# Optimization experiments

Hardware: AMD Instinct MI355X
Metric: run time of the kernel (lower is better)

## Reference

```python
import jax, jax.numpy as jnp
import numpy as np

EMBED_DIM = 128
FFN_DIM = 512
N_NODES = 50000
N_EDGES = 800000
LN_EPS = 1e-5


def setup_inputs() -> dict:
    key = jax.random.key(0)
    ks = jax.random.split(key, 8)
    s = 1.0 / np.sqrt(EMBED_DIM)
    return {
        "x": jax.random.normal(ks[0], (N_NODES, EMBED_DIM), jnp.float32),
        "edge_indices": jax.random.randint(ks[1], (2, N_EDGES), 0, N_NODES, dtype=jnp.int32),
        "W_qkv": jax.random.normal(ks[2], (EMBED_DIM, 3 * EMBED_DIM), jnp.float32) * s,
        "b_qkv": jnp.zeros((3 * EMBED_DIM,), jnp.float32),
        "W1": jax.random.normal(ks[3], (EMBED_DIM, FFN_DIM), jnp.float32) * s,
        "b1": jnp.zeros((FFN_DIM,), jnp.float32),
        "W2": jax.random.normal(ks[4], (FFN_DIM, EMBED_DIM), jnp.float32) * (1.0 / np.sqrt(FFN_DIM)),
        "b2": jnp.zeros((EMBED_DIM,), jnp.float32),
        "g1": jnp.ones((EMBED_DIM,), jnp.float32),
        "be1": jnp.zeros((EMBED_DIM,), jnp.float32),
        "g2": jnp.ones((EMBED_DIM,), jnp.float32),
        "be2": jnp.zeros((EMBED_DIM,), jnp.float32),
    }


def _layernorm(x, g, b):
    mu = jnp.mean(x, axis=-1, keepdims=True)
    var = jnp.mean(jnp.square(x - mu), axis=-1, keepdims=True)
    return (x - mu) * jax.lax.rsqrt(var + LN_EPS) * g + b


def _self_attention(x, edge_indices, W_qkv, b_qkv):
    n = x.shape[0]
    scale = x.shape[1] ** (-0.5)
    qkv = x @ W_qkv + b_qkv
    q, k, v = jnp.split(qkv, 3, axis=1)
    src, dst = edge_indices[0], edge_indices[1]  # row (softmax segment), col
    # per-edge logits: [E]
    alpha = jnp.sum(q[src] * k[dst], axis=1) * scale
    # segment (per-row) stable softmax
    m = jax.ops.segment_max(alpha, src, num_segments=n)
    e = jnp.exp(alpha - m[src])
    denom = jax.ops.segment_sum(e, src, num_segments=n)
    w = e / denom[src]  # [E]
    # sparse.mm: out[i] = sum_{(i,j) in E} w_ij * v[j]
    return jax.ops.segment_sum(w[:, None] * v[dst], src, num_segments=n)


def reference(x, edge_indices, W_qkv, b_qkv, W1, b1, W2, b2, g1, be1, g2, be2):
    # norm_first = False (post-norm), dropout = 0
    x = _layernorm(x + _self_attention(x, edge_indices, W_qkv, b_qkv), g1, be1)
    h = jax.nn.relu(x @ W1 + b1) @ W2 + b2
    x = _layernorm(x + h, g2, be2)
    return x
```

## Files before the change

### kernel.cpp

```cpp
#include <hip/hip_runtime.h>
#include <math.h>

#define NN 50000
#define NE 800000
#define ED 128
#define FD 512
#define MAXDEG 64
#define CURS_STRIDE 16
#define QKV_BLOCKS (NN / 16)
#define SCAT_BLOCKS ((NE + 255) / 256)

typedef __attribute__((ext_vector_type(8))) short bf16x8;
typedef __attribute__((ext_vector_type(4))) float f32x4;
typedef _Float16 half2_t __attribute__((ext_vector_type(2)));

static __device__ __forceinline__ float wave_sum(float x) {
#pragma unroll
  for (int off = 32; off > 0; off >>= 1) x += __shfl_xor(x, off, 64);
  return x;
}

static __device__ __forceinline__ unsigned short f2bf(float f) {
  union { float f; unsigned u; } c; c.f = f;
  unsigned r = c.u + 0x7fffu + ((c.u >> 16) & 1u);
  return (unsigned short)(r >> 16);
}

static __device__ __forceinline__ unsigned short f2h(float f) {
  union { _Float16 h; unsigned short u; } c; c.h = (_Float16)f;
  return c.u;
}

static __device__ __forceinline__ half2_t u2h2(unsigned u) {
  union { unsigned u; half2_t h; } c; c.u = u;
  return c.h;
}

#if __has_builtin(__builtin_amdgcn_fdot2)
#define FDOT2(a, b, c) __builtin_amdgcn_fdot2((a), (b), (c), false)
#else
static __device__ __forceinline__ float FDOT2(half2_t a, half2_t b, float c) {
  return (float)a[0] * (float)b[0] + (float)a[1] * (float)b[1] + c;
}
#endif

__global__ void k_prep(const float* __restrict__ Wqkv, const float* __restrict__ W1,
                       const float* __restrict__ W2, unsigned short* __restrict__ WqkvF,
                       unsigned short* __restrict__ W1F, unsigned short* __restrict__ W2F,
                       int* __restrict__ cursor) {
  int idx = blockIdx.x * 256 + threadIdx.x;
  if (idx < NN) cursor[idx * CURS_STRIDE] = 0;
  if (idx < 49152) {
    int j = idx & 7, l = (idx >> 3) & 63, kb = (idx >> 9) & 3, t = idx >> 11;
    int k = kb * 32 + (l >> 4) * 8 + j, n = t * 16 + (l & 15);
    WqkvF[idx] = f2bf(Wqkv[k * 384 + n]);
  }
  {
    int j = idx & 7, l = (idx >> 3) & 63, kb = (idx >> 9) & 3, t = idx >> 11;
    int k = kb * 32 + (l >> 4) * 8 + j, n = t * 16 + (l & 15);
    W1F[idx] = f2bf(W1[k * 512 + n]);
  }
  {
    int j = idx & 7, l = (idx >> 3) & 63, kb = (idx >> 9) & 15, t = idx >> 13;
    int k = kb * 32 + (l >> 4) * 8 + j, n = t * 16 + (l & 15);
    W2F[idx] = f2bf(W2[k * 128 + n]);
  }
}

__global__ __launch_bounds__(256) void k_qkv_scat(
    const float* __restrict__ X, const unsigned short* __restrict__ WqkvF,
    const float* __restrict__ B, unsigned short* __restrict__ q,
    unsigned short* __restrict__ kv, const int* __restrict__ src,
    const int* __restrict__ dst, int* __restrict__ cursor,
    unsigned short* __restrict__ colidx) {
  __shared__ unsigned short xs[16][136];
  const int tid = threadIdx.x;
  if (blockIdx.x & 1) {
    const int e = (blockIdx.x >> 1) * 256 + tid;
    if (e < NE) {
      const int s = src[e];
      const int d = dst[e];
      const int slot = atomicAdd(&cursor[s * CURS_STRIDE], 1);
      if (slot < MAXDEG) colidx[s * MAXDEG + slot] = (unsigned short)d;
    }
    return;
  }
  const int row0 = (blockIdx.x >> 1) * 16;
  for (int idx = tid; idx < 512; idx += 256) {
    int r = idx >> 5, c4 = (idx & 31) << 2;
    float4 val = *(const float4*)&X[(size_t)(row0 + r) * ED + c4];
    xs[r][c4] = f2bf(val.x); xs[r][c4 + 1] = f2bf(val.y);
    xs[r][c4 + 2] = f2bf(val.z); xs[r][c4 + 3] = f2bf(val.w);
  }
  __syncthreads();
  const int wv = tid >> 6, lane = tid & 63;
  const int ln = lane & 15, quad = lane >> 4;
  const int koff = quad * 8;
  bf16x8 a[4];
#pragma unroll
  for (int kb = 0; kb < 4; kb++) a[kb] = *(const bf16x8*)&xs[ln][kb * 32 + koff];
  for (int g = 0; g < 3; g++) {
    const int t0 = wv * 6 + g * 2;
    bf16x8 b[2][4];
#pragma unroll
    for (int j = 0; j < 2; j++)
#pragma unroll
      for (int kb = 0; kb < 4; kb++)
        b[j][kb] = *(const bf16x8*)&WqkvF[(size_t)(((t0 + j) * 4 + kb) * 64 + lane) * 8];
    f32x4 acc[2];
#pragma unroll
    for (int j = 0; j < 2; j++) acc[j] = (f32x4){0.f, 0.f, 0.f, 0.f};
#pragma unroll
    for (int kb = 0; kb < 4; kb++)
#pragma unroll
      for (int j = 0; j < 2; j++)
        acc[j] = __builtin_amdgcn_mfma_f32_16x16x32_bf16(a[kb], b[j][kb], acc[j], 0, 0, 0);
#pragma unroll
    for (int j = 0; j < 2; j++) {
      const int col = (t0 + j) * 16 + ln;
      const float bias = B[col];
      if (col < 128) {
#pragma unroll
        for (int r = 0; r < 4; r++)
          q[(size_t)(row0 + quad * 4 + r) * ED + col] =
              f2h((acc[j][r] + bias) * 0.08838834764831845f);
      } else {
#pragma unroll
        for (int r = 0; r < 4; r++)
          kv[(size_t)(row0 + quad * 4 + r) * 256 + (col - 128)] = f2h(acc[j][r] + bias);
      }
    }
  }
}

template <bool FULL>
static __device__ __forceinline__ void attn_chunk(
    int base, int cnt, int grp, int gl, int lane, const half2_t* qh,
    const unsigned short* __restrict__ kv, const unsigned short* __restrict__ colidx,
    float& l, half2_t* axh) {
  const int C = FULL ? 16 : cnt;
  int colreg = 0;
  if (lane < C) colreg = colidx[base + lane];
  const int itmax = FULL ? 4 : ((C + 3) >> 2);
#pragma unroll(FULL ? 4 : 1)
  for (int it = 0; it < itmax; it++) {
    const int t = it * 4 + grp;
    const bool act = FULL || t < C;
    const int cc = __shfl(colreg, act ? t : 0, 64);
    const unsigned short* row = &kv[(size_t)cc * 256 + gl * 8];
    uint4 kw = *(const uint4*)row;
    uint4 vw = *(const uint4*)(row + 128);
    float dot = FDOT2(qh[0], u2h2(kw.x), 0.f);
    dot = FDOT2(qh[1], u2h2(kw.y), dot);
    dot = FDOT2(qh[2], u2h2(kw.z), dot);
    dot = FDOT2(qh[3], u2h2(kw.w), dot);
    dot += __shfl_xor(dot, 1, 64);
    dot += __shfl_xor(dot, 2, 64);
    dot += __shfl_xor(dot, 4, 64);
    dot += __shfl_xor(dot, 8, 64);
    const float e = act ? __expf(dot) : 0.f;
    l += e;
    const half2_t e2 = {(_Float16)e, (_Float16)e};
    axh[0] += e2 * u2h2(vw.x);
    axh[1] += e2 * u2h2(vw.y);
    axh[2] += e2 * u2h2(vw.z);
    axh[3] += e2 * u2h2(vw.w);
  }
}

__global__ __launch_bounds__(256) void k_attn(
    const unsigned short* __restrict__ q, const unsigned short* __restrict__ kv,
    const float* __restrict__ x, const int* __restrict__ cursor,
    const unsigned short* __restrict__ colidx, unsigned short* __restrict__ attb) {
  const int wv = threadIdx.x >> 6;
  const int lane = threadIdx.x & 63;
  const int grp = lane >> 4, gl = lane & 15;
  const int node = blockIdx.x * 4 + wv;

  half2_t qh[4];
  {
    uint4 qw = *(const uint4*)&q[(size_t)node * ED + gl * 8];
    qh[0] = u2h2(qw.x); qh[1] = u2h2(qw.y);
    qh[2] = u2h2(qw.z); qh[3] = u2h2(qw.w);
  }
  const int cnt0 = cursor[node * CURS_STRIDE];
  const int cnt = cnt0 > MAXDEG ? MAXDEG : cnt0;
  const int b0 = node * MAXDEG;
  float l = 0.f;
  half2_t axh[4] = {};
  int off = 0;
  for (; off + 16 <= cnt; off += 16)
    attn_chunk<true>(b0 + off, 16, grp, gl, lane, qh, kv, colidx, l, axh);
  if (off < cnt)
    attn_chunk<false>(b0 + off, cnt - off, grp, gl, lane, qh, kv, colidx, l, axh);

#pragma unroll
  for (int j = 0; j < 4; j++) {
    union { half2_t h; int i; } c;
    union { int i; half2_t h; } d;
    c.h = axh[j]; d.i = __shfl_xor(c.i, 16, 64); axh[j] += d.h;
    c.h = axh[j]; d.i = __shfl_xor(c.i, 32, 64); axh[j] += d.h;
  }
  l += __shfl_xor(l, 16, 64);
  l += __shfl_xor(l, 32, 64);

  const float inv = (cnt > 0) ? 1.0f / l : 0.f;
  const int d0 = gl * 8 + grp * 2;
  const half2_t s = (grp == 0) ? axh[0] : (grp == 1) ? axh[1] : (grp == 2) ? axh[2] : axh[3];
  float2 xv = *(const float2*)&x[(size_t)node * ED + d0];
  unsigned pk = (unsigned)f2h(xv.x + (float)s[0] * inv) |
                ((unsigned)f2h(xv.y + (float)s[1] * inv) << 16);
  *(unsigned*)&attb[(size_t)node * ED + d0] = pk;
}

__global__ __launch_bounds__(256) void k_ffn_ln2(
    const unsigned short* __restrict__ attb, const unsigned short* __restrict__ W1F,
    const float* __restrict__ b1, const unsigned short* __restrict__ W2F,
    const float* __restrict__ b2, const float* __restrict__ g1,
    const float* __restrict__ be1, const float* __restrict__ g2,
    const float* __restrict__ be2, float* __restrict__ out) {
  __shared__ unsigned short xs[16][136];
  __shared__ unsigned short hs[16][520];
  __shared__ float ysf[16][132];
  float* ys = (float*)&hs[0][0];
  const int row0 = blockIdx.x * 16;
  const int tid = threadIdx.x;
  {
    const int r = tid >> 4, c8 = (tid & 15) << 3;
    uint4 aw = *(const uint4*)&attb[(size_t)(row0 + r) * ED + c8];
    half2_t h0 = u2h2(aw.x), h1 = u2h2(aw.y), h2 = u2h2(aw.z), h3 = u2h2(aw.w);
    ysf[r][c8] = (float)h0[0];     ysf[r][c8 + 1] = (float)h0[1];
    ysf[r][c8 + 2] = (float)h1[0]; ysf[r][c8 + 3] = (float)h1[1];
    ysf[r][c8 + 4] = (float)h2[0]; ysf[r][c8 + 5] = (float)h2[1];
    ysf[r][c8 + 6] = (float)h3[0]; ysf[r][c8 + 7] = (float)h3[1];
  }
  __syncthreads();
  const int wv = tid >> 6, lane = tid & 63;
#pragma unroll
  for (int half = 0; half < 2; half++) {
    const int r = wv * 4 + half * 2 + (lane >> 5);
    const int hd = (lane & 31) << 2;
    float4 vv = *(const float4*)&ysf[r][hd];
    float s4 = vv.x + vv.y + vv.z + vv.w;
#pragma unroll
    for (int off = 16; off > 0; off >>= 1) s4 += __shfl_xor(s4, off, 64);
    const float mean = s4 * (1.f / ED);
    const float dx0 = vv.x - mean, dx1 = vv.y - mean, dx2 = vv.z - mean, dx3 = vv.w - mean;
    float vr = dx0 * dx0 + dx1 * dx1 + dx2 * dx2 + dx3 * dx3;
#pragma unroll
    for (int off = 16; off > 0; off >>= 1) vr += __shfl_xor(vr, off, 64);
    const float rstd = rsqrtf(vr * (1.f / ED) + 1e-5f);
    const float4 gg = *(const float4*)&g1[hd];
    const float4 bb = *(const float4*)&be1[hd];
    const float o0 = dx0 * rstd * gg.x + bb.x;
    const float o1 = dx1 * rstd * gg.y + bb.y;
    const float o2 = dx2 * rstd * gg.z + bb.z;
    const float o3 = dx3 * rstd * gg.w + bb.w;
    xs[r][hd] = f2bf(o0); xs[r][hd + 1] = f2bf(o1);
    xs[r][hd + 2] = f2bf(o2); xs[r][hd + 3] = f2bf(o3);
    *(float4*)&ysf[r][hd] = make_float4(o0, o1, o2, o3);
  }
  __syncthreads();
  const int ln = lane & 15, quad = lane >> 4;
  const int koff = quad * 8;
  bf16x8 a1[4];
#pragma unroll
  for (int kb = 0; kb < 4; kb++) a1[kb] = *(const bf16x8*)&xs[ln][kb * 32 + koff];
  for (int g = 0; g < 4; g++) {
    const int t0 = wv * 8 + g * 2;
    bf16x8 b[2][4];
#pragma unroll
    for (int j = 0; j < 2; j++)
#pragma unroll
      for (int kb = 0; kb < 4; kb++)
        b[j][kb] = *(const bf16x8*)&W1F[(size_t)(((t0 + j) * 4 + kb) * 64 + lane) * 8];
    f32x4 acc[2];
#pragma unroll
    for (int j = 0; j < 2; j++) acc[j] = (f32x4){0.f, 0.f, 0.f, 0.f};
#pragma unroll
    for (int kb = 0; kb < 4; kb++)
#pragma unroll
      for (int j = 0; j < 2; j++)
        acc[j] = __builtin_amdgcn_mfma_f32_16x16x32_bf16(a1[kb], b[j][kb], acc[j], 0, 0, 0);
#pragma unroll
    for (int j = 0; j < 2; j++) {
      const int col = (t0 + j) * 16 + ln;
      const float bias = b1[col];
#pragma unroll
      for (int r = 0; r < 4; r++)
        hs[quad * 4 + r][col] = f2bf(fmaxf(acc[j][r] + bias, 0.f));
    }
  }
  __syncthreads();
  f32x4 acc2[2];
  acc2[0] = (f32x4){0.f, 0.f, 0.f, 0.f};
  acc2[1] = (f32x4){0.f, 0.f, 0.f, 0.f};
  const int nt0 = wv * 2;
  for (int kg = 0; kg < 4; kg++) {
    bf16x8 a[4];
#pragma unroll
    for (int kk = 0; kk < 4; kk++)
      a[kk] = *(const bf16x8*)&hs[ln][(kg * 4 + kk) * 32 + koff];
    bf16x8 b[2][4];
#pragma unroll
    for (int nt = 0; nt < 2; nt++)
#pragma unroll
      for (int kk = 0; kk < 4; kk++)
        b[nt][kk] = *(const bf16x8*)&W2F[(size_t)(((nt0 + nt) * 16 + kg * 4 + kk) * 64 + lane) * 8];
#pragma unroll
    for (int kk = 0; kk < 4; kk++)
#pragma unroll
      for (int nt = 0; nt < 2; nt++)
        acc2[nt] = __builtin_amdgcn_mfma_f32_16x16x32_bf16(a[kk], b[nt][kk], acc2[nt], 0, 0, 0);
  }
  __syncthreads();
#pragma unroll
  for (int nt = 0; nt < 2; nt++) {
    const int col = (nt0 + nt) * 16 + ln;
    const float bias = b2[col];
#pragma unroll
    for (int r = 0; r < 4; r++)
      ys[(quad * 4 + r) * 132 + col] = acc2[nt][r] + bias;
  }
  __syncthreads();
  float2 gg = *(const float2*)&g2[2 * lane];
  float2 bbe = *(const float2*)&be2[2 * lane];
#pragma unroll
  for (int rr = 0; rr < 4; rr++) {
    const int r = wv * 4 + rr;
    const int row = row0 + r;
    float vx = ys[r * 132 + 2 * lane] + ysf[r][2 * lane];
    float vy = ys[r * 132 + 2 * lane + 1] + ysf[r][2 * lane + 1];
    float mean = wave_sum(vx + vy) * (1.f / ED);
    float dx = vx - mean, dy = vy - mean;
    float var = wave_sum(dx * dx + dy * dy) * (1.f / ED);
    float rstd = rsqrtf(var + 1e-5f);
    float2 o = make_float2(dx * rstd * gg.x + bbe.x, dy * rstd * gg.y + bbe.y);
    *(float2*)&out[(size_t)row * ED + 2 * lane] = o;
  }
}

extern "C" void kernel_launch(void* const* d_in, const int* in_sizes, int n_in,
                              void* d_out, int out_size, void* d_ws, size_t ws_size,
                              hipStream_t stream) {
  const float* x = (const float*)d_in[0];
  const int* ei = (const int*)d_in[1];
  const float* W_qkv = (const float*)d_in[2];
  const float* b_qkv = (const float*)d_in[3];
  const float* W1 = (const float*)d_in[4];
  const float* b1 = (const float*)d_in[5];
  const float* W2 = (const float*)d_in[6];
  const float* b2 = (const float*)d_in[7];
  const float* g1 = (const float*)d_in[8];
  const float* be1 = (const float*)d_in[9];
  const float* g2 = (const float*)d_in[10];
  const float* be2 = (const float*)d_in[11];
  float* out = (float*)d_out;

  char* ws = (char*)d_ws;
  size_t off = 0;
  auto alloc = [&](size_t bytes) -> char* {
    char* p = ws + off;
    off = (off + bytes + 255) & ~(size_t)255;
    return p;
  };
  unsigned short* q = (unsigned short*)alloc(2 * (size_t)NN * ED);
  unsigned short* kv = (unsigned short*)alloc(2 * (size_t)NN * 256);
  unsigned short* attb = (unsigned short*)alloc(2 * (size_t)NN * ED);
  unsigned short* WqkvF = (unsigned short*)alloc(2 * 24 * 4 * 64 * 8);
  unsigned short* W1F = (unsigned short*)alloc(2 * 32 * 4 * 64 * 8);
  unsigned short* W2F = (unsigned short*)alloc(2 * 8 * 16 * 64 * 8);
  int* cursor = (int*)alloc(sizeof(int) * (size_t)NN * CURS_STRIDE);
  unsigned short* colidx = (unsigned short*)alloc(sizeof(unsigned short) * (size_t)NN * MAXDEG);

  k_prep<<<256, 256, 0, stream>>>(W_qkv, W1, W2, WqkvF, W1F, W2F, cursor);
  k_qkv_scat<<<QKV_BLOCKS + SCAT_BLOCKS, 256, 0, stream>>>(x, WqkvF, b_qkv, q, kv,
                                                           ei, ei + NE, cursor, colidx);
  k_attn<<<NN / 4, 256, 0, stream>>>(q, kv, x, cursor, colidx, attb);
  k_ffn_ln2<<<NN / 16, 256, 0, stream>>>(attb, W1F, b1, W2F, b2, g1, be1, g2, be2, out);
}
```

Baseline: 235.7 us.

## Fuse sparse attention into FFN/LayerNorm kernel, keep residual in fp16 LDS

Merges the attention kernel into the FFN+LN2 kernel. Each 16-row block now first computes attention for its 16 nodes, four per wave run sequentially, and writes the residual sum directly to shared memory. This removes the intermediate global buffer and one kernel launch. The LN1 output kept for the second residual is now stored in fp16 in LDS instead of fp32, which cuts shared memory but adds rounding. The trade-off is fewer blocks (NN/16 instead of NN/4) with serialized per-node gather work, which lowers occupancy and latency hiding for the irregular gathers.

```diff
diff --git a/kernel.cpp b/kernel.cpp
--- a/kernel.cpp
+++ b/kernel.cpp
@@ -29,6 +29,11 @@
 static __device__ __forceinline__ unsigned short f2h(float f) {
   union { _Float16 h; unsigned short u; } c; c.h = (_Float16)f;
   return c.u;
+}
+
+static __device__ __forceinline__ float h2f(unsigned short u) {
+  union { unsigned short u; _Float16 h; } c; c.u = u;
+  return (float)c.h;
 }
 
 static __device__ __forceinline__ half2_t u2h2(unsigned u) {
@@ -168,84 +173,72 @@
   }
 }
 
-__global__ __launch_bounds__(256) void k_attn(
+__global__ __launch_bounds__(256) void k_attn_ffn(
     const unsigned short* __restrict__ q, const unsigned short* __restrict__ kv,
     const float* __restrict__ x, const int* __restrict__ cursor,
-    const unsigned short* __restrict__ colidx, unsigned short* __restrict__ attb) {
-  const int wv = threadIdx.x >> 6;
-  const int lane = threadIdx.x & 63;
-  const int grp = lane >> 4, gl = lane & 15;
-  const int node = blockIdx.x * 4 + wv;
-
-  half2_t qh[4];
-  {
-    uint4 qw = *(const uint4*)&q[(size_t)node * ED + gl * 8];
-    qh[0] = u2h2(qw.x); qh[1] = u2h2(qw.y);
-    qh[2] = u2h2(qw.z); qh[3] = u2h2(qw.w);
-  }
-  const int cnt0 = cursor[node * CURS_STRIDE];
-  const int cnt = cnt0 > MAXDEG ? MAXDEG : cnt0;
-  const int b0 = node * MAXDEG;
-  float l = 0.f;
-  half2_t axh[4] = {};
-  int off = 0;
-  for (; off + 16 <= cnt; off += 16)
-    attn_chunk<true>(b0 + off, 16, grp, gl, lane, qh, kv, colidx, l, axh);
-  if (off < cnt)
-    attn_chunk<false>(b0 + off, cnt - off, grp, gl, lane, qh, kv, colidx, l, axh);
-
-#pragma unroll
-  for (int j = 0; j < 4; j++) {
-    union { half2_t h; int i; } c;
-    union { int i; half2_t h; } d;
-    c.h = axh[j]; d.i = __shfl_xor(c.i, 16, 64); axh[j] += d.h;
-    c.h = axh[j]; d.i = __shfl_xor(c.i, 32, 64); axh[j] += d.h;
-  }
-  l += __shfl_xor(l, 16, 64);
-  l += __shfl_xor(l, 32, 64);
-
-  const float inv = (cnt > 0) ? 1.0f / l : 0.f;
-  const int d0 = gl * 8 + grp * 2;
-  const half2_t s = (grp == 0) ? axh[0] : (grp == 1) ? axh[1] : (grp == 2) ? axh[2] : axh[3];
-  float2 xv = *(const float2*)&x[(size_t)node * ED + d0];
-  unsigned pk = (unsigned)f2h(xv.x + (float)s[0] * inv) |
-                ((unsigned)f2h(xv.y + (float)s[1] * inv) << 16);
-  *(unsigned*)&attb[(size_t)node * ED + d0] = pk;
-}
-
-__global__ __launch_bounds__(256) void k_ffn_ln2(
-    const unsigned short* __restrict__ attb, const unsigned short* __restrict__ W1F,
+    const unsigned short* __restrict__ colidx, const unsigned short* __restrict__ W1F,
     const float* __restrict__ b1, const unsigned short* __restrict__ W2F,
     const float* __restrict__ b2, const float* __restrict__ g1,
     const float* __restrict__ be1, const float* __restrict__ g2,
     const float* __restrict__ be2, float* __restrict__ out) {
   __shared__ unsigned short xs[16][136];
   __shared__ unsigned short hs[16][520];
-  __shared__ float ysf[16][132];
+  __shared__ unsigned short ysf[16][136];
   float* ys = (float*)&hs[0][0];
   const int row0 = blockIdx.x * 16;
   const int tid = threadIdx.x;
-  {
-    const int r = tid >> 4, c8 = (tid & 15) << 3;
-    uint4 aw = *(const uint4*)&attb[(size_t)(row0 + r) * ED + c8];
-    half2_t h0 = u2h2(aw.x), h1 = u2h2(aw.y), h2 = u2h2(aw.z), h3 = u2h2(aw.w);
-    ysf[r][c8] = (float)h0[0];     ysf[r][c8 + 1] = (float)h0[1];
-    ysf[r][c8 + 2] = (float)h1[0]; ysf[r][c8 + 3] = (float)h1[1];
-    ysf[r][c8 + 4] = (float)h2[0]; ysf[r][c8 + 5] = (float)h2[1];
-    ysf[r][c8 + 6] = (float)h3[0]; ysf[r][c8 + 7] = (float)h3[1];
-  }
-  __syncthreads();
   const int wv = tid >> 6, lane = tid & 63;
+  const int grp = lane >> 4, gl = lane & 15;
+
+  for (int i = 0; i < 4; i++) {
+    const int node = row0 + wv * 4 + i;
+    half2_t qh[4];
+    {
+      uint4 qw = *(const uint4*)&q[(size_t)node * ED + gl * 8];
+      qh[0] = u2h2(qw.x); qh[1] = u2h2(qw.y);
+      qh[2] = u2h2(qw.z); qh[3] = u2h2(qw.w);
+    }
+    const int cnt0 = cursor[node * CURS_STRIDE];
+    const int cnt = cnt0 > MAXDEG ? MAXDEG : cnt0;
+    const int b0 = node * MAXDEG;
+    float l = 0.f;
+    half2_t axh[4] = {};
+    int off = 0;
+    for (; off + 16 <= cnt; off += 16)
+      attn_chunk<true>(b0 + off, 16, grp, gl, lane, qh, kv, colidx, l, axh);
+    if (off < cnt)
+      attn_chunk<false>(b0 + off, cnt - off, grp, gl, lane, qh, kv, colidx, l, axh);
+#pragma unroll
+    for (int j = 0; j < 4; j++) {
+      union { half2_t h; int i; } c;
+      union { int i; half2_t h; } d;
+      c.h = axh[j]; d.i = __shfl_xor(c.i, 16, 64); axh[j] += d.h;
+      c.h = axh[j]; d.i = __shfl_xor(c.i, 32, 64); axh[j] += d.h;
+    }
+    l += __shfl_xor(l, 16, 64);
+    l += __shfl_xor(l, 32, 64);
+    const float inv = (cnt > 0) ? 1.0f / l : 0.f;
+    const int d0 = gl * 8 + grp * 2;
+    const half2_t s = (grp == 0) ? axh[0] : (grp == 1) ? axh[1] : (grp == 2) ? axh[2] : axh[3];
+    float2 xv = *(const float2*)&x[(size_t)node * ED + d0];
+    unsigned pk = (unsigned)f2h(xv.x + (float)s[0] * inv) |
+                  ((unsigned)f2h(xv.y + (float)s[1] * inv) << 16);
+    *(unsigned*)&ysf[wv * 4 + i][d0] = pk;
+  }
+  __syncthreads();
+
 #pragma unroll
   for (int half = 0; half < 2; half++) {
     const int r = wv * 4 + half * 2 + (lane >> 5);
     const int hd = (lane & 31) << 2;
-    float4 vv = *(const float4*)&ysf[r][hd];
-    float s4 = vv.x + vv.y + vv.z + vv.w;
+    uint2 pv = *(const uint2*)&ysf[r][hd];
+    half2_t a01 = u2h2(pv.x), a23 = u2h2(pv.y);
+    float v0 = (float)a01[0], v1 = (float)a01[1], v2 = (float)a23[0], v3 = (float)a23[1];
+    float s4 = v0 + v1 + v2 + v3;
 #pragma unroll
     for (int off = 16; off > 0; off >>= 1) s4 += __shfl_xor(s4, off, 64);
     const float mean = s4 * (1.f / ED);
-    const float dx0 = vv.x - mean, dx1 = vv.y - mean, dx2 = vv.z - mean, dx3 = vv.w - mean;
+    const float dx0 = v0 - mean, dx1 = v1 - mean, dx2 = v2 - mean, dx3 = v3 - mean;
     float vr = dx0 * dx0 + dx1 * dx1 + dx2 * dx2 + dx3 * dx3;
 #pragma unroll
     for (int off = 16; off > 0; off >>= 1) vr += __shfl_xor(vr, off, 64);
@@ -258,7 +251,8 @@
     const float o3 = dx3 * rstd * gg.w + bb.w;
     xs[r][hd] = f2bf(o0); xs[r][hd + 1] = f2bf(o1);
     xs[r][hd + 2] = f2bf(o2); xs[r][hd + 3] = f2bf(o3);
-    *(float4*)&ysf[r][hd] = make_float4(o0, o1, o2, o3);
+    ysf[r][hd] = f2h(o0); ysf[r][hd + 1] = f2h(o1);
+    ysf[r][hd + 2] = f2h(o2); ysf[r][hd + 3] = f2h(o3);
   }
   __syncthreads();
   const int ln = lane & 15, quad = lane >> 4;
@@ -329,8 +323,8 @@
   for (int rr = 0; rr < 4; rr++) {
     const int r = wv * 4 + rr;
     const int row = row0 + r;
-    float vx = ys[r * 132 + 2 * lane] + ysf[r][2 * lane];
-    float vy = ys[r * 132 + 2 * lane + 1] + ysf[r][2 * lane + 1];
+    float vx = ys[r * 132 + 2 * lane] + h2f(ysf[r][2 * lane]);
+    float vy = ys[r * 132 + 2 * lane + 1] + h2f(ysf[r][2 * lane + 1]);
     float mean = wave_sum(vx + vy) * (1.f / ED);
     float dx = vx - mean, dy = vy - mean;
     float var = wave_sum(dx * dx + dy * dy) * (1.f / ED);
@@ -366,7 +360,6 @@
   };
   unsigned short* q = (unsigned short*)alloc(2 * (size_t)NN * ED);
   unsigned short* kv = (unsigned short*)alloc(2 * (size_t)NN * 256);
-  unsigned short* attb = (unsigned short*)alloc(2 * (size_t)NN * ED);
   unsigned short* WqkvF = (unsigned short*)alloc(2 * 24 * 4 * 64 * 8);
   unsigned short* W1F = (unsigned short*)alloc(2 * 32 * 4 * 64 * 8);
   unsigned short* W2F = (unsigned short*)alloc(2 * 8 * 16 * 64 * 8);
@@ -376,6 +369,6 @@
   k_prep<<<256, 256, 0, stream>>>(W_qkv, W1, W2, WqkvF, W1F, W2F, cursor);
   k_qkv_scat<<<QKV_BLOCKS + SCAT_BLOCKS, 256, 0, stream>>>(x, WqkvF, b_qkv, q, kv,
                                                            ei, ei + NE, cursor, colidx);
-  k_attn<<<NN / 4, 256, 0, stream>>>(q, kv, x, cursor, colidx, attb);
-  k_ffn_ln2<<<NN / 16, 256, 0, stream>>>(attb, W1F, b1, W2F, b2, g1, be1, g2, be2, out);
-}
+  k_attn_ffn<<<NN / 16, 256, 0, stream>>>(q, kv, x, cursor, colidx, W1F, b1, W2F, b2,
+                                          g1, be1, g2, be2, out);
+}
```

New measurement: 241.5 us. +2.5%, slower.
